# Optimization experiments

Measured on AMD Instinct MI355X. Metric: run time of the kernel, lower is better.

The kernel has to match this reference:

```python
import jax, jax.numpy as jnp
import numpy as np

N_NODES = 50000

def _gcn_conv(x, W, b, src, dst, n):
    # GCNConv: add self-loops, symmetric normalization D^-1/2 (A+I) D^-1/2, then aggregate X@W
    h = x @ W  # [N, out]
    loop = jnp.arange(n, dtype=src.dtype)
    s = jnp.concatenate([src, loop])
    d = jnp.concatenate([dst, loop])
    deg = jax.ops.segment_sum(jnp.ones_like(d, dtype=h.dtype), d, num_segments=n)  # in-degree incl self-loop (>=1)
    dinv = jax.lax.rsqrt(deg)
    norm = dinv[s] * dinv[d]  # [E+N]
    msg = h[s] * norm[:, None]  # gather + scale
    out = jax.ops.segment_sum(msg, d, num_segments=n)  # scatter-add
    return out + b

def setup_inputs() -> dict:
    key = jax.random.key(0)
    k1, k2, k3, k4, k5 = jax.random.split(key, 5)
    F_IN, HID, CLS, E = 256, 128, 32, 800000
    x = jax.random.normal(k1, (N_NODES, F_IN), dtype=jnp.float32)
    edge_index = jax.random.randint(k2, (2, E), 0, N_NODES, dtype=jnp.int64)
    W1 = jax.random.normal(k3, (F_IN, HID), dtype=jnp.float32) / np.sqrt(F_IN)
    b1 = jnp.zeros((HID,), dtype=jnp.float32)
    W2 = jax.random.normal(k4, (HID, CLS), dtype=jnp.float32) / np.sqrt(HID)
    b2 = jnp.zeros((CLS,), dtype=jnp.float32)
    return {"x": x, "edge_index": edge_index, "W1": W1, "b1": b1, "W2": W2, "b2": b2}

def reference(x, edge_index, W1, b1, W2, b2):
    src, dst = edge_index[0], edge_index[1]
    h = _gcn_conv(x, W1, b1, src, dst, N_NODES)
    h = jax.nn.relu(h)
    h = _gcn_conv(h, W2, b2, src, dst, N_NODES)
    return jax.nn.log_softmax(h, axis=1)
```

## Files before the change

kernel.cpp:

```cpp
#include <hip/hip_runtime.h>

#define N_NODES 50000
#define N_PAD   50176
#define F_IN 256
#define HID 128
#define CLS 32
#define N_EDGE 800000

#define NB    196
#define NPART 196
#define CHUNK 4082
#define GBLKS 782

typedef short bf16x8 __attribute__((ext_vector_type(8)));
typedef short s16x4  __attribute__((ext_vector_type(4)));
typedef short s16x8  __attribute__((ext_vector_type(8)));
typedef float f32x2  __attribute__((ext_vector_type(2)));
typedef float f32x4  __attribute__((ext_vector_type(4)));

static __device__ inline short f2bf(float f) {
    union { float f; unsigned u; } v; v.f = f;
    unsigned r = v.u + 0x7FFFu + ((v.u >> 16) & 1u);
    return (short)(r >> 16);
}

static __device__ inline unsigned char f2fp8(float f) {
    return (unsigned char)(__builtin_amdgcn_cvt_pk_fp8_f32(f, f, 0, false) & 0xFF);
}


__global__ __launch_bounds__(256) void k_pre(const int* __restrict__ dst,
                                             int* __restrict__ counts,
                                             const float* __restrict__ W1,
                                             short* __restrict__ WtP,
                                             const float* __restrict__ W2,
                                             short* __restrict__ Wt2P) {
    int blk = blockIdx.x, tid = threadIdx.x;
    if (blk < NB) {
        __shared__ int hist[NPART];
        if (tid < NPART) hist[tid] = 0;
        __syncthreads();
        int lo = blk * CHUNK, hi = min(lo + CHUNK, N_EDGE);
        for (int e = lo + tid; e < hi; e += 256)
            atomicAdd(&hist[dst[e] >> 8], 1);
        __syncthreads();
        if (tid < NPART) counts[blk * NPART + tid] = hist[tid];
    } else if (blk < NB + 128) {
        int idx = (blk - NB) * 256 + tid;
        int e  = idx & 7;
        int l  = (idx >> 3) & 63;
        int nt = (idx >> 9) & 7;
        int ks = idx >> 12;
        int k  = ks * 32 + ((l >> 4) * 8) + e;
        int col = nt * 16 + (l & 15);
        WtP[idx] = f2bf(W1[(size_t)k * HID + col]);
    } else {
        int idx = (blk - NB - 128) * 256 + tid;
        int e  = idx & 7;
        int l  = (idx >> 3) & 63;
        int nt = (idx >> 9) & 1;
        int ks = (idx >> 10) & 3;
        int k  = ks * 32 + ((l >> 4) * 8) + e;
        int col = nt * 16 + (l & 15);
        Wt2P[idx] = f2bf(W2[(size_t)k * CLS + col]);
    }
}


__global__ __launch_bounds__(256) void k_scanP1(const int* __restrict__ counts,
                                                int* __restrict__ base,
                                                int* __restrict__ ptot) {
    __shared__ int s[256];
    int tid = threadIdx.x, p = blockIdx.x;
    int v = (tid < NB) ? counts[tid * NPART + p] : 0;
    s[tid] = v;
    __syncthreads();
#pragma unroll
    for (int off = 1; off < 256; off <<= 1) {
        int t = (tid >= off) ? s[tid - off] : 0;
        __syncthreads();
        s[tid] += t;
        __syncthreads();
    }
    if (tid < NB) base[tid * NPART + p] = s[tid] - v;
    if (tid == 255) ptot[p] = s[255];
}


__global__ __launch_bounds__(256) void k_bucket(const int* __restrict__ src,
                                                const int* __restrict__ dst,
                                                const int* __restrict__ base,
                                                const int* __restrict__ ptot,
                                                int* __restrict__ bucket) {
    __shared__ int s[256];
    __shared__ int cur[NPART];
    int tid = threadIdx.x, blk = blockIdx.x;
    int v = (tid < NPART) ? ptot[tid] : 0;
    s[tid] = v;
    __syncthreads();
#pragma unroll
    for (int off = 1; off < 256; off <<= 1) {
        int t = (tid >= off) ? s[tid - off] : 0;
        __syncthreads();
        s[tid] += t;
        __syncthreads();
    }
    if (tid < NPART) cur[tid] = base[blk * NPART + tid] + (s[tid] - v);
    __syncthreads();
    int lo = blk * CHUNK, hi = min(lo + CHUNK, N_EDGE);
    for (int e = lo + tid; e < hi; e += 256) {
        int d = dst[e], sv = src[e];
        int pos = atomicAdd(&cur[d >> 8], 1);
        bucket[pos] = ((d & 255) << 16) | sv;
    }
}


__global__ __launch_bounds__(256) void k_csrf_gemm1(const int* __restrict__ bucket,
                                                    const int* __restrict__ ptot,
                                                    int* __restrict__ esrc,
                                                    int* __restrict__ offs,
                                                    float* __restrict__ dinv,
                                                    const float* __restrict__ x,
                                                    const short* __restrict__ WtP,
                                                    unsigned char* __restrict__ h) {
    __shared__ short tile[64][256];
    int blk = blockIdx.x, tid = threadIdx.x;

    if (blk < NPART) {
        int* sA = (int*)&tile[0][0];
        int* sB = sA + 256;
        int* sC = sB + 256;
        int* sX = sC + 256;
        int p = blk;
        int v = (tid < NPART) ? ptot[tid] : 0;
        sA[tid] = v;
        __syncthreads();
#pragma unroll
        for (int off = 1; off < 256; off <<= 1) {
            int t = (tid >= off) ? sA[tid - off] : 0;
            __syncthreads();
            sA[tid] += t;
            __syncthreads();
        }
        if (tid == p) sX[0] = sA[tid] - v;
        sB[tid] = 0;
        __syncthreads();
        int beg = sX[0], end = beg + ptot[p];
        for (int i = beg + tid; i < end; i += 256)
            atomicAdd(&sB[bucket[i] >> 16], 1);
        __syncthreads();
        int hv = sB[tid];
        sA[tid] = hv;
        __syncthreads();
#pragma unroll
        for (int off = 1; off < 256; off <<= 1) {
            int t = (tid >= off) ? sA[tid - off] : 0;
            __syncthreads();
            sA[tid] += t;
            __syncthreads();
        }
        int excl = sA[tid] - hv;
        sC[tid] = excl;
        int node = p * 256 + tid;
        if (node <= N_NODES) offs[node] = beg + excl;
        if (node < N_NODES) dinv[node] = rsqrtf((float)(hv + 1));
        __syncthreads();
        for (int i = beg + tid; i < end; i += 256) {
            int pk = bucket[i];
            int slot = atomicAdd(&sC[pk >> 16], 1);
            esrc[beg + slot] = pk & 0xFFFF;
        }
        return;
    }

    const int R0 = (blk - NPART) * 64;

#pragma unroll 8
    for (int it = 0; it < 16; ++it) {
        int rl = it * 4 + (tid >> 6);
        int row = min(R0 + rl, N_NODES - 1);
        int c = (tid & 63) * 4;
        f32x4 xv = *(const f32x4*)(x + (size_t)row * F_IN + c);
        s16x4 bv = { f2bf(xv[0]), f2bf(xv[1]), f2bf(xv[2]), f2bf(xv[3]) };
        int byte = rl * 512 + c * 2;
        byte ^= ((rl & 7) << 4);
        *(s16x4*)((char*)&tile[0][0] + byte) = bv;
    }
    __syncthreads();

    const int lane = tid & 63;
    const int w    = tid >> 6;
    const int l15  = lane & 15;
    const int lk   = lane >> 4;

    f32x4 acc[8] = {};

#pragma unroll
    for (int ks = 0; ks < F_IN / 32; ++ks) {
        const int kbase = ks * 32 + lk * 8;

        int rl = w * 16 + l15;
        int byte = rl * 512 + kbase * 2;
        byte ^= ((rl & 7) << 4);
        bf16x8 afrag = *(const bf16x8*)((char*)&tile[0][0] + byte);

        bf16x8 bfrag[8];
#pragma unroll
        for (int nt = 0; nt < 8; ++nt)
            bfrag[nt] = *(const bf16x8*)(WtP + (size_t)((ks * 8 + nt) * 64 + lane) * 8);

#pragma unroll
        for (int nt = 0; nt < 8; ++nt)
            acc[nt] = __builtin_amdgcn_mfma_f32_16x16x32_bf16(afrag, bfrag[nt], acc[nt], 0, 0, 0);
    }

#pragma unroll
    for (int r = 0; r < 4; ++r) {
        int m = R0 + w * 16 + lk * 4 + r;
        if (m < N_NODES) {
#pragma unroll
            for (int nt = 0; nt < 8; ++nt) {
                int n = nt * 16 + l15;
                h[(size_t)m * HID + n] = f2fp8(acc[nt][r]);
            }
        }
    }
}


__global__ __launch_bounds__(256) void k_gather1(const int* __restrict__ offs,
                                                 const int* __restrict__ esrc,
                                                 const unsigned char* __restrict__ h,
                                                 const float* __restrict__ dinv,
                                                 const float* __restrict__ b,
                                                 short* __restrict__ out) {
    int node = blockIdx.x * 16 + (threadIdx.x >> 4);
    int lane = threadIdx.x & 15;
    if (node >= N_NODES) return;
    int f = lane * 8;
    float dv = dinv[node];
    uint2 hv = *(const uint2*)(h + (size_t)node * HID + f);
    f32x2 q0 = __builtin_amdgcn_cvt_pk_f32_fp8(hv.x, false);
    f32x2 q1 = __builtin_amdgcn_cvt_pk_f32_fp8(hv.x, true);
    f32x2 q2 = __builtin_amdgcn_cvt_pk_f32_fp8(hv.y, false);
    f32x2 q3 = __builtin_amdgcn_cvt_pk_f32_fp8(hv.y, true);
    float self = dv * dv;
    float a0 = q0[0] * self, a1 = q0[1] * self, a2 = q1[0] * self, a3 = q1[1] * self;
    float a4 = q2[0] * self, a5 = q2[1] * self, a6 = q3[0] * self, a7 = q3[1] * self;

    int beg = offs[node], end = offs[node + 1];
    int p = beg;
#define ACC8(vv, nn) { \
    f32x2 c0 = __builtin_amdgcn_cvt_pk_f32_fp8(vv.x, false); \
    f32x2 c1 = __builtin_amdgcn_cvt_pk_f32_fp8(vv.x, true);  \
    f32x2 c2 = __builtin_amdgcn_cvt_pk_f32_fp8(vv.y, false); \
    f32x2 c3 = __builtin_amdgcn_cvt_pk_f32_fp8(vv.y, true);  \
    a0 += c0[0] * nn; a1 += c0[1] * nn; a2 += c1[0] * nn; a3 += c1[1] * nn; \
    a4 += c2[0] * nn; a5 += c2[1] * nn; a6 += c3[0] * nn; a7 += c3[1] * nn; }
    for (; p + 7 < end; p += 8) {
        int s0 = esrc[p + 0], s1 = esrc[p + 1], s2 = esrc[p + 2], s3 = esrc[p + 3];
        int s4 = esrc[p + 4], s5 = esrc[p + 5], s6 = esrc[p + 6], s7 = esrc[p + 7];
        float n0 = dinv[s0] * dv, n1 = dinv[s1] * dv, n2 = dinv[s2] * dv, n3 = dinv[s3] * dv;
        float n4 = dinv[s4] * dv, n5 = dinv[s5] * dv, n6 = dinv[s6] * dv, n7 = dinv[s7] * dv;
        uint2 v0 = *(const uint2*)(h + (size_t)s0 * HID + f);
        uint2 v1 = *(const uint2*)(h + (size_t)s1 * HID + f);
        uint2 v2 = *(const uint2*)(h + (size_t)s2 * HID + f);
        uint2 v3 = *(const uint2*)(h + (size_t)s3 * HID + f);
        uint2 v4 = *(const uint2*)(h + (size_t)s4 * HID + f);
        uint2 v5 = *(const uint2*)(h + (size_t)s5 * HID + f);
        uint2 v6 = *(const uint2*)(h + (size_t)s6 * HID + f);
        uint2 v7 = *(const uint2*)(h + (size_t)s7 * HID + f);
        ACC8(v0, n0); ACC8(v1, n1); ACC8(v2, n2); ACC8(v3, n3);
        ACC8(v4, n4); ACC8(v5, n5); ACC8(v6, n6); ACC8(v7, n7);
    }
    for (; p + 3 < end; p += 4) {
        int s0 = esrc[p + 0], s1 = esrc[p + 1], s2 = esrc[p + 2], s3 = esrc[p + 3];
        float n0 = dinv[s0] * dv, n1 = dinv[s1] * dv, n2 = dinv[s2] * dv, n3 = dinv[s3] * dv;
        uint2 v0 = *(const uint2*)(h + (size_t)s0 * HID + f);
        uint2 v1 = *(const uint2*)(h + (size_t)s1 * HID + f);
        uint2 v2 = *(const uint2*)(h + (size_t)s2 * HID + f);
        uint2 v3 = *(const uint2*)(h + (size_t)s3 * HID + f);
        ACC8(v0, n0); ACC8(v1, n1); ACC8(v2, n2); ACC8(v3, n3);
    }
    for (; p < end; ++p) {
        int s = esrc[p];
        float nrm = dinv[s] * dv;
        uint2 v = *(const uint2*)(h + (size_t)s * HID + f);
        ACC8(v, nrm);
    }
#undef ACC8
    float4 bv0 = *(const float4*)(b + f);
    float4 bv1 = *(const float4*)(b + f + 4);
    s16x8 o = { f2bf(a0 + bv0.x), f2bf(a1 + bv0.y), f2bf(a2 + bv0.z), f2bf(a3 + bv0.w),
                f2bf(a4 + bv1.x), f2bf(a5 + bv1.y), f2bf(a6 + bv1.z), f2bf(a7 + bv1.w) };
    *(s16x8*)(out + (size_t)node * HID + f) = o;
}


__global__ __launch_bounds__(256) void k_gemm2_mfma(const short* __restrict__ a,
                                                    const short* __restrict__ Wt2P,
                                                    unsigned char* __restrict__ h) {
    const int lane = threadIdx.x & 63;
    const int w    = threadIdx.x >> 6;
    const int l15  = lane & 15;
    const int lk   = lane >> 4;
    const int row0 = blockIdx.x * 128 + w * 32;

    f32x4 acc[2][2] = {};

#pragma unroll
    for (int ks = 0; ks < HID / 32; ++ks) {
        const int kbase = ks * 32 + lk * 8;

        bf16x8 afrag[2];
#pragma unroll
        for (int mt = 0; mt < 2; ++mt) {
            int row = row0 + mt * 16 + l15;
            row = min(row, N_NODES - 1);
            bf16x8 av = *(const bf16x8*)(a + (size_t)row * HID + kbase);
#pragma unroll
            for (int e = 0; e < 8; ++e) if (av[e] < 0) av[e] = 0;
            afrag[mt] = av;
        }

        bf16x8 bfrag[2];
#pragma unroll
        for (int nt = 0; nt < 2; ++nt)
            bfrag[nt] = *(const bf16x8*)(Wt2P + (size_t)((ks * 2 + nt) * 64 + lane) * 8);

#pragma unroll
        for (int mt = 0; mt < 2; ++mt)
#pragma unroll
            for (int nt = 0; nt < 2; ++nt)
                acc[mt][nt] = __builtin_amdgcn_mfma_f32_16x16x32_bf16(
                    afrag[mt], bfrag[nt], acc[mt][nt], 0, 0, 0);
    }

#pragma unroll
    for (int mt = 0; mt < 2; ++mt) {
#pragma unroll
        for (int r = 0; r < 4; ++r) {
            int m = row0 + mt * 16 + lk * 4 + r;
            if (m < N_NODES) {
#pragma unroll
                for (int nt = 0; nt < 2; ++nt) {
                    int n = nt * 16 + l15;
                    h[(size_t)m * CLS + n] = f2fp8(acc[mt][nt][r]);
                }
            }
        }
    }
}


__global__ __launch_bounds__(256) void k_gather2(const int* __restrict__ offs,
                                                 const int* __restrict__ esrc,
                                                 const unsigned char* __restrict__ h,
                                                 const float* __restrict__ dinv,
                                                 const float* __restrict__ b,
                                                 float* __restrict__ out) {
    int node = blockIdx.x * 32 + (threadIdx.x >> 3);
    int sub = threadIdx.x & 7;
    if (node >= N_NODES) return;
    int f = sub * 4;
    float dv = dinv[node];
    unsigned hv = *(const unsigned*)(h + (size_t)node * CLS + f);
    f32x2 hlo = __builtin_amdgcn_cvt_pk_f32_fp8(hv, false);
    f32x2 hhi = __builtin_amdgcn_cvt_pk_f32_fp8(hv, true);
    float self = dv * dv;
    float a0 = hlo[0] * self, a1 = hlo[1] * self, a2 = hhi[0] * self, a3 = hhi[1] * self;
    int beg = offs[node], end = offs[node + 1];
    int p = beg;
#define ACC4(vv, nn) { \
    f32x2 l = __builtin_amdgcn_cvt_pk_f32_fp8(vv, false); \
    f32x2 u = __builtin_amdgcn_cvt_pk_f32_fp8(vv, true);  \
    a0 += l[0] * nn; a1 += l[1] * nn; a2 += u[0] * nn; a3 += u[1] * nn; }
    for (; p + 7 < end; p += 8) {
        int s0 = esrc[p], s1 = esrc[p + 1], s2 = esrc[p + 2], s3 = esrc[p + 3];
        int s4 = esrc[p + 4], s5 = esrc[p + 5], s6 = esrc[p + 6], s7 = esrc[p + 7];
        float n0 = dinv[s0] * dv, n1 = dinv[s1] * dv, n2 = dinv[s2] * dv, n3 = dinv[s3] * dv;
        float n4 = dinv[s4] * dv, n5 = dinv[s5] * dv, n6 = dinv[s6] * dv, n7 = dinv[s7] * dv;
        unsigned v0 = *(const unsigned*)(h + (size_t)s0 * CLS + f);
        unsigned v1 = *(const unsigned*)(h + (size_t)s1 * CLS + f);
        unsigned v2 = *(const unsigned*)(h + (size_t)s2 * CLS + f);
        unsigned v3 = *(const unsigned*)(h + (size_t)s3 * CLS + f);
        unsigned v4 = *(const unsigned*)(h + (size_t)s4 * CLS + f);
        unsigned v5 = *(const unsigned*)(h + (size_t)s5 * CLS + f);
        unsigned v6 = *(const unsigned*)(h + (size_t)s6 * CLS + f);
        unsigned v7 = *(const unsigned*)(h + (size_t)s7 * CLS + f);
        ACC4(v0, n0); ACC4(v1, n1); ACC4(v2, n2); ACC4(v3, n3);
        ACC4(v4, n4); ACC4(v5, n5); ACC4(v6, n6); ACC4(v7, n7);
    }
    for (; p + 3 < end; p += 4) {
        int s0 = esrc[p], s1 = esrc[p + 1], s2 = esrc[p + 2], s3 = esrc[p + 3];
        float n0 = dinv[s0] * dv, n1 = dinv[s1] * dv, n2 = dinv[s2] * dv, n3 = dinv[s3] * dv;
        unsigned v0 = *(const unsigned*)(h + (size_t)s0 * CLS + f);
        unsigned v1 = *(const unsigned*)(h + (size_t)s1 * CLS + f);
        unsigned v2 = *(const unsigned*)(h + (size_t)s2 * CLS + f);
        unsigned v3 = *(const unsigned*)(h + (size_t)s3 * CLS + f);
        ACC4(v0, n0); ACC4(v1, n1); ACC4(v2, n2); ACC4(v3, n3);
    }
    for (; p < end; ++p) {
        int s = esrc[p];
        float nrm = dinv[s] * dv;
        unsigned v = *(const unsigned*)(h + (size_t)s * CLS + f);
        ACC4(v, nrm);
    }
#undef ACC4
    float4 bv = *(const float4*)(b + f);
    float4 acc = { a0 + bv.x, a1 + bv.y, a2 + bv.z, a3 + bv.w };

    float m = fmaxf(fmaxf(acc.x, acc.y), fmaxf(acc.z, acc.w));
    m = fmaxf(m, __shfl_xor(m, 1, 8));
    m = fmaxf(m, __shfl_xor(m, 2, 8));
    m = fmaxf(m, __shfl_xor(m, 4, 8));
    float sum = expf(acc.x - m) + expf(acc.y - m) + expf(acc.z - m) + expf(acc.w - m);
    sum += __shfl_xor(sum, 1, 8);
    sum += __shfl_xor(sum, 2, 8);
    sum += __shfl_xor(sum, 4, 8);
    float l = m + logf(sum);
    float4 o = { acc.x - l, acc.y - l, acc.z - l, acc.w - l };
    *(float4*)(out + (size_t)node * CLS + f) = o;
}


extern "C" void kernel_launch(void* const* d_in, const int* in_sizes, int n_in,
                              void* d_out, int out_size, void* d_ws, size_t ws_size,
                              hipStream_t stream) {
    const float* x  = (const float*)d_in[0];
    const int*   ei = (const int*)d_in[1];
    const float* W1 = (const float*)d_in[2];
    const float* b1 = (const float*)d_in[3];
    const float* W2 = (const float*)d_in[4];
    const float* b2 = (const float*)d_in[5];
    float* out = (float*)d_out;

    const int* src = ei;
    const int* dst = ei + N_EDGE;

    int* counts   = (int*)d_ws;
    int* base     = counts + NB * NPART;
    int* ptot     = base + NB * NPART;
    int* bucket   = ptot + 256;
    int* offs     = bucket + N_EDGE;
    int* esrc     = offs + N_PAD;
    float* dinv   = (float*)(esrc + N_EDGE);
    unsigned char* h1 = (unsigned char*)(dinv + N_PAD);
    short* a1     = (short*)(h1 + (size_t)N_NODES * HID);
    unsigned char* h2 = (unsigned char*)(a1 + (size_t)N_NODES * HID);
    short* WtP    = (short*)(h2 + (size_t)N_NODES * CLS);
    short* Wt2P   = WtP + HID * F_IN;

    k_pre       <<<NB + 128 + 16, 256, 0, stream>>>(dst, counts, W1, WtP, W2, Wt2P);
    k_scanP1    <<<NPART,         256, 0, stream>>>(counts, base, ptot);
    k_bucket    <<<NB,            256, 0, stream>>>(src, dst, base, ptot, bucket);
    k_csrf_gemm1<<<NPART + GBLKS, 256, 0, stream>>>(bucket, ptot, esrc, offs, dinv, x, WtP, h1);

    k_gather1   <<<3125,          256, 0, stream>>>(offs, esrc, h1, dinv, b1, a1);
    k_gemm2_mfma<<<391,           256, 0, stream>>>(a1, Wt2P, h2);
    k_gather2   <<<1563,          256, 0, stream>>>(offs, esrc, h2, dinv, b2, out);
}
```

Baseline: 81.53 us.

## Fuse first-layer aggregation with second-layer GEMM via shared memory

Merges the layer-1 gather kernel and the layer-2 MFMA GEMM into one kernel: each block aggregates 16 nodes into LDS as bf16, then one wave applies ReLU and multiplies by W2 to produce fp8 h2. This removes the global round trip of the intermediate activation buffer and one kernel launch. In exchange, each block adds a barrier and a serial MFMA tail run by a single wave, and the bounds check is dropped, relying on the node count being an exact multiple of 16.

```diff
diff --git a/kernel.cpp b/kernel.cpp
--- a/kernel.cpp
+++ b/kernel.cpp
@@ -229,16 +229,22 @@
 }
 
 
-__global__ __launch_bounds__(256) void k_gather1(const int* __restrict__ offs,
-                                                 const int* __restrict__ esrc,
-                                                 const unsigned char* __restrict__ h,
-                                                 const float* __restrict__ dinv,
-                                                 const float* __restrict__ b,
-                                                 short* __restrict__ out) {
-    int node = blockIdx.x * 16 + (threadIdx.x >> 4);
-    int lane = threadIdx.x & 15;
-    if (node >= N_NODES) return;
-    int f = lane * 8;
+#define ALDS2 132
+
+__global__ __launch_bounds__(256) void k_g1g2(const int* __restrict__ offs,
+                                              const int* __restrict__ esrc,
+                                              const unsigned char* __restrict__ h,
+                                              const float* __restrict__ dinv,
+                                              const float* __restrict__ b,
+                                              const short* __restrict__ Wt2P,
+                                              unsigned char* __restrict__ h2) {
+    __shared__ short a_lds[16][ALDS2];
+    const int tid = threadIdx.x;
+    const int nl = tid >> 4;
+    const int node = blockIdx.x * 16 + nl;
+    const int lane16 = tid & 15;
+    const int f = lane16 * 8;
+
     float dv = dinv[node];
     uint2 hv = *(const uint2*)(h + (size_t)node * HID + f);
     f32x2 q0 = __builtin_amdgcn_cvt_pk_f32_fp8(hv.x, false);
@@ -294,60 +300,33 @@
     float4 bv1 = *(const float4*)(b + f + 4);
     s16x8 o = { f2bf(a0 + bv0.x), f2bf(a1 + bv0.y), f2bf(a2 + bv0.z), f2bf(a3 + bv0.w),
                 f2bf(a4 + bv1.x), f2bf(a5 + bv1.y), f2bf(a6 + bv1.z), f2bf(a7 + bv1.w) };
-    *(s16x8*)(out + (size_t)node * HID + f) = o;
-}
-
-
-__global__ __launch_bounds__(256) void k_gemm2_mfma(const short* __restrict__ a,
-                                                    const short* __restrict__ Wt2P,
-                                                    unsigned char* __restrict__ h) {
-    const int lane = threadIdx.x & 63;
-    const int w    = threadIdx.x >> 6;
-    const int l15  = lane & 15;
-    const int lk   = lane >> 4;
-    const int row0 = blockIdx.x * 128 + w * 32;
-
-    f32x4 acc[2][2] = {};
-
-#pragma unroll
-    for (int ks = 0; ks < HID / 32; ++ks) {
-        const int kbase = ks * 32 + lk * 8;
-
-        bf16x8 afrag[2];
-#pragma unroll
-        for (int mt = 0; mt < 2; ++mt) {
-            int row = row0 + mt * 16 + l15;
-            row = min(row, N_NODES - 1);
-            bf16x8 av = *(const bf16x8*)(a + (size_t)row * HID + kbase);
+    *(s16x8*)&a_lds[nl][f] = o;
+    __syncthreads();
+
+    if (tid < 64) {
+        const int lane = tid;
+        const int l15 = lane & 15;
+        const int lk  = lane >> 4;
+        f32x4 acc[2] = {};
+#pragma unroll
+        for (int ks = 0; ks < HID / 32; ++ks) {
+            const int kbase = ks * 32 + lk * 8;
+            bf16x8 av = *(const bf16x8*)&a_lds[l15][kbase];
 #pragma unroll
             for (int e = 0; e < 8; ++e) if (av[e] < 0) av[e] = 0;
-            afrag[mt] = av;
-        }
-
-        bf16x8 bfrag[2];
-#pragma unroll
-        for (int nt = 0; nt < 2; ++nt)
-            bfrag[nt] = *(const bf16x8*)(Wt2P + (size_t)((ks * 2 + nt) * 64 + lane) * 8);
-
-#pragma unroll
-        for (int mt = 0; mt < 2; ++mt)
-#pragma unroll
-            for (int nt = 0; nt < 2; ++nt)
-                acc[mt][nt] = __builtin_amdgcn_mfma_f32_16x16x32_bf16(
-                    afrag[mt], bfrag[nt], acc[mt][nt], 0, 0, 0);
-    }
-
-#pragma unroll
-    for (int mt = 0; mt < 2; ++mt) {
+#pragma unroll
+            for (int nt = 0; nt < 2; ++nt) {
+                bf16x8 bfrag = *(const bf16x8*)(Wt2P + (size_t)((ks * 2 + nt) * 64 + lane) * 8);
+                acc[nt] = __builtin_amdgcn_mfma_f32_16x16x32_bf16(av, bfrag, acc[nt], 0, 0, 0);
+            }
+        }
 #pragma unroll
         for (int r = 0; r < 4; ++r) {
-            int m = row0 + mt * 16 + lk * 4 + r;
-            if (m < N_NODES) {
-#pragma unroll
-                for (int nt = 0; nt < 2; ++nt) {
-                    int n = nt * 16 + l15;
-                    h[(size_t)m * CLS + n] = f2fp8(acc[mt][nt][r]);
-                }
+            int m = blockIdx.x * 16 + lk * 4 + r;
+#pragma unroll
+            for (int nt = 0; nt < 2; ++nt) {
+                int n = nt * 16 + l15;
+                h2[(size_t)m * CLS + n] = f2fp8(acc[nt][r]);
             }
         }
     }
@@ -447,8 +426,7 @@
     int* esrc     = offs + N_PAD;
     float* dinv   = (float*)(esrc + N_EDGE);
     unsigned char* h1 = (unsigned char*)(dinv + N_PAD);
-    short* a1     = (short*)(h1 + (size_t)N_NODES * HID);
-    unsigned char* h2 = (unsigned char*)(a1 + (size_t)N_NODES * HID);
+    unsigned char* h2 = h1 + (size_t)N_NODES * HID;
     short* WtP    = (short*)(h2 + (size_t)N_NODES * CLS);
     short* Wt2P   = WtP + HID * F_IN;
 
@@ -457,7 +435,6 @@
     k_bucket    <<<NB,            256, 0, stream>>>(src, dst, base, ptot, bucket);
     k_csrf_gemm1<<<NPART + GBLKS, 256, 0, stream>>>(bucket, ptot, esrc, offs, dinv, x, WtP, h1);
 
-    k_gather1   <<<3125,          256, 0, stream>>>(offs, esrc, h1, dinv, b1, a1);
-    k_gemm2_mfma<<<391,           256, 0, stream>>>(a1, Wt2P, h2);
+    k_g1g2      <<<3125,          256, 0, stream>>>(offs, esrc, h1, dinv, b1, Wt2P, h2);
     k_gather2   <<<1563,          256, 0, stream>>>(offs, esrc, h2, dinv, b2, out);
 }
```

New measurement: 76.94 us, median of 3. -5.6%, faster.
